# Kernel tuning notes

Measured on AMD Instinct MI355X. Metric: run time of the kernel, lower is better.

The kernel has to match this reference:

```python
import jax, jax.numpy as jnp
import numpy as np

N_NODES, F_IN, HID, HEADS, REP, NCLS = 8192, 128, 64, 8, 512, 32
E, NSYN, LMAX = 2048, 4096, 8
DM, DI, DSTATE, DCONV, DTR = 512, 1024, 16, 4, 32


def setup_inputs():
    key = jax.random.key(0)
    ks = jax.random.split(key, 24)
    g = lambda i, shape, s=0.05: jax.random.normal(ks[i], shape, jnp.float32) * s
    return {
        "edge_attr": jax.random.normal(ks[0], (E, 8), jnp.float32),
        "synapse": jax.random.normal(ks[1], (NSYN, 6), jnp.float32),
        "x_param": g(2, (N_NODES, F_IN), 0.1),
        "W1": g(3, (F_IN, HEADS * HID)),
        "att_src1": g(4, (HEADS, HID), 0.1),
        "att_dst1": g(5, (HEADS, HID), 0.1),
        "b1": jnp.zeros((HEADS * HID,), jnp.float32),
        "W2": g(6, (HEADS * HID, REP)),
        "att_src2": g(7, (1, REP), 0.1),
        "att_dst2": g(8, (1, REP), 0.1),
        "b2": jnp.zeros((REP,), jnp.float32),
        "W_in": g(9, (6, DM), 0.1),
        "b_in": jnp.zeros((DM,), jnp.float32),
        "W_inproj": g(10, (DM, 2 * DI)),
        "conv_w": g(11, (DI, DCONV), 0.1),
        "conv_b": jnp.zeros((DI,), jnp.float32),
        "W_xproj": g(12, (DI, DTR + 2 * DSTATE)),
        "W_dt": g(13, (DTR, DI), 0.1),
        "b_dt": jnp.full((DI,), -4.0, jnp.float32),
        "A_log": jnp.log(jnp.tile(jnp.arange(1, DSTATE + 1, dtype=jnp.float32), (DI, 1))),
        "D": jnp.ones((DI,), jnp.float32),
        "W_outproj": g(14, (DI, DM)),
        "W_lout": g(15, (DM, DM)),
        "b_lout": jnp.zeros((DM,), jnp.float32),
        "Wc1": g(16, (REP + 2 * DM, 512)),
        "bc1": jnp.zeros((512,), jnp.float32),
        "Wc2": g(17, (512, NCLS)),
        "bc2": jnp.zeros((NCLS,), jnp.float32),
        "edge_index": jax.random.randint(ks[18], (2, E), 0, N_NODES),
        "synapse_index": jnp.sort(jax.random.randint(ks[19], (NSYN,), 0, E)),
        "scatter_size": N_NODES,
    }


def _gat(x, W, a_src, a_dst, bias, src, dst, heads, out_ch, concat):
    # PyG GATConv (eval mode, edge_dim=None, self-loops already appended to src/dst)
    n = x.shape[0]
    xw = (x @ W).reshape(n, heads, out_ch)
    e = (xw * a_src).sum(-1)[src] + (xw * a_dst).sum(-1)[dst]  # [E+N, H]
    e = jax.nn.leaky_relu(e, 0.2)
    m = jax.ops.segment_max(e, dst, num_segments=n)
    ex = jnp.exp(e - m[dst])
    denom = jax.ops.segment_sum(ex, dst, num_segments=n)
    alpha = ex / denom[dst]
    out = jax.ops.segment_sum(alpha[:, :, None] * xw[src], dst, num_segments=n)
    out = out.reshape(n, heads * out_ch) if concat else out.mean(1)
    return out + bias


def _mamba_encoder(synapse, synapse_index, W_in, b_in, W_inproj, conv_w, conv_b,
                   W_xproj, W_dt, b_dt, A_log, D, W_outproj, W_lout, b_lout):
    # ragged [NSYN,6] -> padded [E, LMAX, 6] (synapse_index is sorted)
    counts = jax.ops.segment_sum(jnp.ones((NSYN,), jnp.int32), synapse_index, num_segments=E)
    starts = jnp.cumsum(counts) - counts
    pos = jnp.arange(NSYN) - starts[synapse_index]
    padded = jnp.zeros((E, LMAX, synapse.shape[1]), synapse.dtype).at[
        synapse_index, pos].set(synapse, mode="drop")
    u = padded @ W_in + b_in                     # linear_in: [E, L, DM]
    xz = u @ W_inproj                            # in_proj:   [E, L, 2*DI]
    xm, z = xz[..., :DI], xz[..., DI:]
    # depthwise causal conv over time
    xc = jax.lax.conv_general_dilated(
        xm.transpose(0, 2, 1), conv_w[:, None, :],
        window_strides=(1,), padding=[(DCONV - 1, 0)],
        dimension_numbers=("NCH", "OIH", "NCH"), feature_group_count=DI)
    xc = jax.nn.silu(xc + conv_b[:, None]).transpose(0, 2, 1)  # [E, L, DI]
    xdb = xc @ W_xproj
    dt = jax.nn.softplus(xdb[..., :DTR] @ W_dt + b_dt)         # [E, L, DI]
    Bm = xdb[..., DTR:DTR + DSTATE]                            # [E, L, N]
    Cm = xdb[..., DTR + DSTATE:]                               # [E, L, N]
    A = -jnp.exp(A_log)                                        # [DI, N]

    def step(h, t):
        dt_t, B_t, C_t, x_t = t                                # [E,DI],[E,N],[E,N],[E,DI]
        h = jnp.exp(dt_t[:, :, None] * A) * h + (dt_t * x_t)[:, :, None] * B_t[:, None, :]
        return h, jnp.einsum("bdn,bn->bd", h, C_t)

    h0 = jnp.zeros((E, DI, DSTATE), xc.dtype)
    _, ys = jax.lax.scan(step, h0, (dt.transpose(1, 0, 2), Bm.transpose(1, 0, 2),
                                    Cm.transpose(1, 0, 2), xc.transpose(1, 0, 2)))
    y = ys.transpose(1, 0, 2) + D * xc                         # [E, L, DI]
    out = (y * jax.nn.silu(z)) @ W_outproj                     # [E, L, DM]
    # masked mean over true sequence length (empty groups behave like a zero seq of len 1)
    cnt = jnp.clip(counts, 1, LMAX).astype(out.dtype)
    mask = (jnp.arange(LMAX)[None, :] < cnt[:, None]).astype(out.dtype)
    pooled = (out * mask[:, :, None]).sum(1) / cnt[:, None]
    return pooled @ W_lout + b_lout                            # [E, DM]


def _forward(edge_attr, synapse, x_param, W1, att_src1, att_dst1, b1,
             W2, att_src2, att_dst2, b2, W_in, b_in, W_inproj, conv_w, conv_b,
             W_xproj, W_dt, b_dt, A_log, D, W_outproj, W_lout, b_lout,
             Wc1, bc1, Wc2, bc2, edge_index, synapse_index, scatter_size):
    # GAT stack (eval: dropouts identity; edge_attr unused since edge_dim=None)
    loops = jnp.arange(N_NODES)
    src = jnp.concatenate([edge_index[0], loops])
    dst = jnp.concatenate([edge_index[1], loops])
    h = jax.nn.elu(_gat(x_param, W1, att_src1, att_dst1, b1, src, dst, HEADS, HID, True))
    h = _gat(h, W2, att_src2, att_dst2, b2, src, dst, 1, REP, False)   # [N, REP]
    x_point = _mamba_encoder(synapse, synapse_index, W_in, b_in, W_inproj, conv_w,
                             conv_b, W_xproj, W_dt, b_dt, A_log, D, W_outproj,
                             W_lout, b_lout)                            # [E, DM]

    def smax(idx):
        s = jax.ops.segment_max(x_point, idx, num_segments=scatter_size)
        nz = jax.ops.segment_sum(jnp.ones((E,), jnp.int32), idx, num_segments=scatter_size)
        return jnp.where(nz[:, None] > 0, s, 0.0)  # torch_scatter: empty slots -> 0

    left, right = smax(edge_index[0]), smax(edge_index[1])
    feats = jnp.concatenate([h, left, right], axis=1)          # [N, REP+2*DM]
    return jax.nn.relu(feats @ Wc1 + bc1) @ Wc2 + bc2          # [N, NCLS]


def reference(edge_attr, synapse, x_param, W1, att_src1, att_dst1, b1,
              W2, att_src2, att_dst2, b2, W_in, b_in, W_inproj, conv_w, conv_b,
              W_xproj, W_dt, b_dt, A_log, D, W_outproj, W_lout, b_lout,
              Wc1, bc1, Wc2, bc2, edge_index, synapse_index, scatter_size):
    return _forward(edge_attr, synapse, x_param, W1, att_src1, att_dst1, b1,
                    W2, att_src2, att_dst2, b2, W_in, b_in, W_inproj, conv_w, conv_b,
                    W_xproj, W_dt, b_dt, A_log, D, W_outproj, W_lout, b_lout,
                    Wc1, bc1, Wc2, bc2, edge_index, synapse_index, scatter_size)
```

## Files before the change

kernel.cpp:

```cpp
#include <hip/hip_runtime.h>

#define N_NODES 8192
#define F_IN 128
#define HID 64
#define HEADS 8
#define REP 512
#define NCLS 32
#define E_EDGES 2048
#define NSYN 4096
#define LMAX 8
#define DM 512
#define DI 1024
#define DSTATE 16
#define DCONV 4
#define DTR 32
#define TOT_EDGES (E_EDGES + N_NODES)
#define ROWS (E_EDGES * LMAX)
#define MC_CAP 6144

typedef short bf16x8 __attribute__((ext_vector_type(8)));
typedef float f32x4 __attribute__((ext_vector_type(4)));

__device__ __forceinline__ unsigned mapf(float f) {
  unsigned u = __float_as_uint(f);
  return (u & 0x80000000u) ? ~u : (u | 0x80000000u);
}
__device__ __forceinline__ float unmapf(unsigned u) {
  return __uint_as_float((u & 0x80000000u) ? (u ^ 0x80000000u) : ~u);
}
__device__ __forceinline__ float fsig(float x) {
  return __builtin_amdgcn_rcpf(1.0f + __expf(-x));
}
__device__ __forceinline__ float fsoftplus(float x) {
  return fmaxf(x, 0.0f) + __logf(1.0f + __expf(-fabsf(x)));
}
__device__ __forceinline__ unsigned short f2bf(float f) {
  unsigned u = __float_as_uint(f);
  unsigned r = (u + 0x7FFFu + ((u >> 16) & 1u)) >> 16;
  return (unsigned short)r;
}
__device__ __forceinline__ float bf2f(unsigned short h) {
  return __uint_as_float(((unsigned)h) << 16);
}
__device__ __forceinline__ void split2(float x, unsigned short* hh, unsigned short* ll) {
  unsigned short h = f2bf(x);
  *hh = h;
  *ll = f2bf(x - bf2f(h));
}
__device__ __forceinline__ int lower_bound_dev(const int* __restrict__ arr, int n, int v) {
  int lo = 0, hi = n;
  while (lo < hi) { int mid = (lo + hi) >> 1; if (arr[mid] < v) lo = mid + 1; else hi = mid; }
  return lo;
}
__device__ __forceinline__ int src_of(const int* __restrict__ ei, int i) {
  return i < E_EDGES ? ei[i] : i - E_EDGES;
}
__device__ __forceinline__ int dst_of(const int* __restrict__ ei, int i) {
  return i < E_EDGES ? ei[E_EDGES + i] : i - E_EDGES;
}
__device__ __forceinline__ int clip_cnt(int c) { return c < 1 ? 1 : (c > LMAX ? LMAX : c); }

__global__ __launch_bounds__(512) void gemm_mfma2(
    const unsigned short* __restrict__ Ah, const unsigned short* __restrict__ Al,
    const unsigned short* __restrict__ Bth, const unsigned short* __restrict__ Btl,
    float* __restrict__ C, int M, int N, int K,
    const float* __restrict__ bias, int act) {
  __shared__ __align__(16) unsigned short As[2][128][40];
  __shared__ __align__(16) unsigned short Bs[2][128][40];
  const int tid = threadIdx.x;
  const int w = tid >> 6;
  const int lane = tid & 63;
  const int wr = w >> 2, wc = w & 3;
  const int mb = M >> 7;
  const int lin = blockIdx.x;
  const int bx = lin / mb;
  const int by = lin % mb;
  const int brow = by * 128;
  const int bcol = bx * 128;
  const int r0 = lane & 15;
  const int kg = lane >> 4;
  const int row0 = tid >> 2, kc0 = tid & 3;
  const size_t a0 = (size_t)(brow + row0) * K + kc0 * 8;
  const size_t b0 = (size_t)(bcol + row0) * K + kc0 * 8;
  f32x4 acc[4][2] = {};
  {
    bf16x8 t0 = *(const bf16x8*)(Ah + a0), t1 = *(const bf16x8*)(Al + a0);
    bf16x8 t2 = *(const bf16x8*)(Bth + b0), t3 = *(const bf16x8*)(Btl + b0);
    *(bf16x8*)(&As[0][row0][kc0 * 8]) = t0;
    *(bf16x8*)(&As[1][row0][kc0 * 8]) = t1;
    *(bf16x8*)(&Bs[0][row0][kc0 * 8]) = t2;
    *(bf16x8*)(&Bs[1][row0][kc0 * 8]) = t3;
  }
  __syncthreads();
  for (int kt = 0; kt < K; kt += 32) {
    const bool more = (kt + 32) < K;
    bf16x8 p0, p1, p2, p3;
    if (more) {
      p0 = *(const bf16x8*)(Ah + a0 + kt + 32);
      p1 = *(const bf16x8*)(Al + a0 + kt + 32);
      p2 = *(const bf16x8*)(Bth + b0 + kt + 32);
      p3 = *(const bf16x8*)(Btl + b0 + kt + 32);
    }
    bf16x8 bhv[2], blv[2];
#pragma unroll
    for (int cf = 0; cf < 2; ++cf) {
      bhv[cf] = *(const bf16x8*)(&Bs[0][wc * 32 + cf * 16 + r0][kg * 8]);
      blv[cf] = *(const bf16x8*)(&Bs[1][wc * 32 + cf * 16 + r0][kg * 8]);
    }
#pragma unroll
    for (int rf = 0; rf < 4; ++rf) {
      bf16x8 ah = *(const bf16x8*)(&As[0][wr * 64 + rf * 16 + r0][kg * 8]);
      bf16x8 al = *(const bf16x8*)(&As[1][wr * 64 + rf * 16 + r0][kg * 8]);
#pragma unroll
      for (int cf = 0; cf < 2; ++cf) {
        acc[rf][cf] = __builtin_amdgcn_mfma_f32_16x16x32_bf16(ah, bhv[cf], acc[rf][cf], 0, 0, 0);
        acc[rf][cf] = __builtin_amdgcn_mfma_f32_16x16x32_bf16(ah, blv[cf], acc[rf][cf], 0, 0, 0);
        acc[rf][cf] = __builtin_amdgcn_mfma_f32_16x16x32_bf16(al, bhv[cf], acc[rf][cf], 0, 0, 0);
      }
    }
    __syncthreads();
    if (more) {
      *(bf16x8*)(&As[0][row0][kc0 * 8]) = p0;
      *(bf16x8*)(&As[1][row0][kc0 * 8]) = p1;
      *(bf16x8*)(&Bs[0][row0][kc0 * 8]) = p2;
      *(bf16x8*)(&Bs[1][row0][kc0 * 8]) = p3;
    }
    __syncthreads();
  }
#pragma unroll
  for (int rf = 0; rf < 4; ++rf)
#pragma unroll
    for (int cf = 0; cf < 2; ++cf) {
      int col = bcol + wc * 32 + cf * 16 + r0;
      float bb = bias ? bias[col] : 0.0f;
#pragma unroll
      for (int j = 0; j < 4; ++j) {
        int row = brow + wr * 64 + rf * 16 + kg * 4 + j;
        float v = acc[rf][cf][j] + bb;
        if (act == 1) v = fmaxf(v, 0.0f);
        C[(size_t)row * N + col] = v;
      }
    }
}

__global__ __launch_bounds__(256) void gemm_mfma_sk(
    const unsigned short* __restrict__ Ah, const unsigned short* __restrict__ Al,
    const unsigned short* __restrict__ Bth, const unsigned short* __restrict__ Btl,
    float* __restrict__ C, int M, int N, int K) {
  __shared__ __align__(16) unsigned short As[2][64][40];
  const int tid = threadIdx.x;
  const int w = tid >> 6;
  const int lane = tid & 63;
  const int brow = blockIdx.y * 64;
  const int bcol = blockIdx.x * 64;
  const int srow = tid >> 2;
  const int skc = tid & 3;
  const int r0 = lane & 15;
  const int kg = lane >> 4;
  const int kchunk = K / gridDim.z;
  const int k0 = blockIdx.z * kchunk;
  f32x4 acc[4] = {};
  const size_t aoff = (size_t)(brow + srow) * K;
  const size_t boff = (size_t)(bcol + w * 16 + r0) * K + kg * 8;
  for (int kt = k0; kt < k0 + kchunk; kt += 32) {
    bf16x8 bh = *(const bf16x8*)(Bth + boff + kt);
    bf16x8 bl = *(const bf16x8*)(Btl + boff + kt);
    *(bf16x8*)(&As[0][srow][skc * 8]) = *(const bf16x8*)(Ah + aoff + kt + skc * 8);
    *(bf16x8*)(&As[1][srow][skc * 8]) = *(const bf16x8*)(Al + aoff + kt + skc * 8);
    __syncthreads();
#pragma unroll
    for (int r = 0; r < 4; ++r) {
      bf16x8 ah = *(const bf16x8*)(&As[0][r * 16 + r0][kg * 8]);
      bf16x8 al = *(const bf16x8*)(&As[1][r * 16 + r0][kg * 8]);
      acc[r] = __builtin_amdgcn_mfma_f32_16x16x32_bf16(ah, bh, acc[r], 0, 0, 0);
      acc[r] = __builtin_amdgcn_mfma_f32_16x16x32_bf16(ah, bl, acc[r], 0, 0, 0);
      acc[r] = __builtin_amdgcn_mfma_f32_16x16x32_bf16(al, bh, acc[r], 0, 0, 0);
    }
    __syncthreads();
  }
  const int col = bcol + w * 16 + r0;
#pragma unroll
  for (int r = 0; r < 4; ++r) {
#pragma unroll
    for (int j = 0; j < 4; ++j) {
      int row = brow + r * 16 + kg * 4 + j;
      atomicAdd(&C[(size_t)row * N + col], acc[r][j]);
    }
  }
}

template <int APPLY_RELU>
__global__ __launch_bounds__(256) void gemm_thin32(
    const float* __restrict__ A32,
    const unsigned short* __restrict__ Bth, const unsigned short* __restrict__ Btl,
    float* __restrict__ C, int M, const float* __restrict__ bias) {
  const int tid = threadIdx.x;
  const int w = tid >> 6;
  const int lane = tid & 63;
  const int r0 = lane & 15;
  const int kg = lane >> 4;
  const int rowbase = blockIdx.x * 64 + w * 16;
  f32x4 acc[2] = {};
  const float* arow = A32 + (size_t)(rowbase + r0) * 512 + kg * 8;
  for (int kt = 0; kt < 512; kt += 32) {
    float4 f0 = *(const float4*)(arow + kt);
    float4 f1 = *(const float4*)(arow + kt + 4);
    float v[8] = {f0.x, f0.y, f0.z, f0.w, f1.x, f1.y, f1.z, f1.w};
    bf16x8 ah, al;
#pragma unroll
    for (int j = 0; j < 8; ++j) {
      float vv = APPLY_RELU ? fmaxf(v[j], 0.0f) : v[j];
      unsigned short hh, ll;
      split2(vv, &hh, &ll);
      ah[j] = (short)hh;
      al[j] = (short)ll;
    }
#pragma unroll
    for (int cf = 0; cf < 2; ++cf) {
      bf16x8 bh = *(const bf16x8*)(Bth + (size_t)(cf * 16 + r0) * 512 + kt + kg * 8);
      bf16x8 bl = *(const bf16x8*)(Btl + (size_t)(cf * 16 + r0) * 512 + kt + kg * 8);
      acc[cf] = __builtin_amdgcn_mfma_f32_16x16x32_bf16(ah, bh, acc[cf], 0, 0, 0);
      acc[cf] = __builtin_amdgcn_mfma_f32_16x16x32_bf16(ah, bl, acc[cf], 0, 0, 0);
      acc[cf] = __builtin_amdgcn_mfma_f32_16x16x32_bf16(al, bh, acc[cf], 0, 0, 0);
    }
  }
#pragma unroll
  for (int cf = 0; cf < 2; ++cf) {
    int col = cf * 16 + r0;
    float bb = bias[col];
#pragma unroll
    for (int j = 0; j < 4; ++j) {
      int row = rowbase + kg * 4 + j;
      C[(size_t)row * 32 + col] = acc[cf][j] + bb;
    }
  }
}

__global__ void split_kernel(const float* __restrict__ x, unsigned short* __restrict__ h,
                             unsigned short* __restrict__ l, int n) {
  int i = blockIdx.x * 256 + threadIdx.x;
  if (i >= n) return;
  split2(x[i], &h[i], &l[i]);
}

__global__ void tsplit_kernel(const float* __restrict__ W, unsigned short* __restrict__ Wth,
                              unsigned short* __restrict__ Wtl, int K, int N) {
  int i = blockIdx.x * 256 + threadIdx.x;
  if (i >= K * N) return;
  int k = i / N, n = i - k * N;
  float v = W[i];
  unsigned short h = f2bf(v);
  Wth[(size_t)n * K + k] = h;
  Wtl[(size_t)n * K + k] = f2bf(v - bf2f(h));
}

#define PREP_SEG0 262144
#define PREP_SEG1 524288
#define PREP_SEG2 16384
#define PREP_SEG3 65536
#define PREP_SEG4 65536
#define PREP_SEG5 1048576
#define PREP_TOT (PREP_SEG0 + PREP_SEG1 + PREP_SEG2 + PREP_SEG3 + PREP_SEG4 + PREP_SEG5)
__global__ void prep1_kernel(
    const float* __restrict__ W_lout, const float* __restrict__ W_outproj,
    const float* __restrict__ A_log, const float* __restrict__ W_xproj,
    const float* __restrict__ W1, const float* __restrict__ x_param,
    unsigned short* __restrict__ Wlth, unsigned short* __restrict__ Wltl,
    unsigned short* __restrict__ Woph, unsigned short* __restrict__ Wopl,
    float* __restrict__ negA,
    unsigned short* __restrict__ Wxth, unsigned short* __restrict__ Wxtl,
    unsigned short* __restrict__ W1th, unsigned short* __restrict__ W1tl,
    unsigned short* __restrict__ xph, unsigned short* __restrict__ xpl) {
  int i = blockIdx.x * 256 + threadIdx.x;
  if (i < PREP_SEG0) {
    int k = i >> 9, n = i & 511;
    float v = W_lout[i];
    unsigned short h = f2bf(v);
    Wlth[(size_t)n * 512 + k] = h;
    Wltl[(size_t)n * 512 + k] = f2bf(v - bf2f(h));
    return;
  }
  i -= PREP_SEG0;
  if (i < PREP_SEG1) { split2(W_outproj[i], &Woph[i], &Wopl[i]); return; }
  i -= PREP_SEG1;
  if (i < PREP_SEG2) { negA[i] = -__expf(A_log[i]); return; }
  i -= PREP_SEG2;
  if (i < PREP_SEG3) {
    int k = i >> 6, n = i & 63;
    float v = W_xproj[i];
    unsigned short h = f2bf(v);
    Wxth[(size_t)n * 1024 + k] = h;
    Wxtl[(size_t)n * 1024 + k] = f2bf(v - bf2f(h));
    return;
  }
  i -= PREP_SEG3;
  if (i < PREP_SEG4) {
    int k = i >> 9, n = i & 511;
    float v = W1[i];
    unsigned short h = f2bf(v);
    W1th[(size_t)n * 128 + k] = h;
    W1tl[(size_t)n * 128 + k] = f2bf(v - bf2f(h));
    return;
  }
  i -= PREP_SEG4;
  if (i < PREP_SEG5) { split2(x_param[i], &xph[i], &xpl[i]); }
}

template <int BM, int BN>
__global__ __launch_bounds__(256) void gemm_t(
    const float* __restrict__ A, int lda,
    const float* __restrict__ B, int ldb,
    float* __restrict__ C, int ldc,
    int M, int N, int K,
    const float* __restrict__ bias, int act) {
  constexpr int RR = BM / 64;
  constexpr int CR = BN / 64;
  __shared__ float As[16][BM + 4];
  __shared__ float Bs[16][BN + 4];
  const int tid = threadIdx.x;
  const int tx = tid & 15;
  const int ty = tid >> 4;
  const int brow = blockIdx.y * BM;
  const int bcol = blockIdx.x * BN;
  float acc[RR][CR][4][4] = {};
  for (int kt = 0; kt < K; kt += 16) {
#pragma unroll
    for (int p = 0; p < RR; ++p) {
      int c = tid + p * 256;
      int row = c >> 2, kc = c & 3;
      int gr = brow + row;
      float4 v = make_float4(0.f, 0.f, 0.f, 0.f);
      if (gr < M) v = *reinterpret_cast<const float4*>(A + (size_t)gr * lda + kt + kc * 4);
      As[kc * 4 + 0][row] = v.x;
      As[kc * 4 + 1][row] = v.y;
      As[kc * 4 + 2][row] = v.z;
      As[kc * 4 + 3][row] = v.w;
    }
#pragma unroll
    for (int p = 0; p < CR; ++p) {
      int c = tid + p * 256;
      int k = c / (BN / 4), c4 = c % (BN / 4);
      int gc = bcol + c4 * 4;
      float4 v = make_float4(0.f, 0.f, 0.f, 0.f);
      if (gc < N) v = *reinterpret_cast<const float4*>(B + (size_t)(kt + k) * ldb + gc);
      *reinterpret_cast<float4*>(&Bs[k][c4 * 4]) = v;
    }
    __syncthreads();
#pragma unroll
    for (int k = 0; k < 16; ++k) {
      float av[RR * 4], bv[CR * 4];
#pragma unroll
      for (int r = 0; r < RR; ++r) {
        float4 t = *reinterpret_cast<const float4*>(&As[k][r * 64 + ty * 4]);
        av[r * 4 + 0] = t.x; av[r * 4 + 1] = t.y; av[r * 4 + 2] = t.z; av[r * 4 + 3] = t.w;
      }
#pragma unroll
      for (int cq = 0; cq < CR; ++cq) {
        float4 t = *reinterpret_cast<const float4*>(&Bs[k][cq * 64 + tx * 4]);
        bv[cq * 4 + 0] = t.x; bv[cq * 4 + 1] = t.y; bv[cq * 4 + 2] = t.z; bv[cq * 4 + 3] = t.w;
      }
#pragma unroll
      for (int r = 0; r < RR; ++r)
#pragma unroll
        for (int cq = 0; cq < CR; ++cq)
#pragma unroll
          for (int i = 0; i < 4; ++i)
#pragma unroll
            for (int j = 0; j < 4; ++j)
              acc[r][cq][i][j] = fmaf(av[r * 4 + i], bv[cq * 4 + j], acc[r][cq][i][j]);
    }
    __syncthreads();
  }
#pragma unroll
  for (int r = 0; r < RR; ++r)
#pragma unroll
    for (int i = 0; i < 4; ++i) {
      int row = brow + r * 64 + ty * 4 + i;
      if (row >= M) continue;
#pragma unroll
      for (int cq = 0; cq < CR; ++cq) {
        int col = bcol + cq * 64 + tx * 4;
        if (col >= N) continue;
        float4 v;
        v.x = acc[r][cq][i][0]; v.y = acc[r][cq][i][1];
        v.z = acc[r][cq][i][2]; v.w = acc[r][cq][i][3];
        if (bias) {
          float4 bb = *reinterpret_cast<const float4*>(bias + col);
          v.x += bb.x; v.y += bb.y; v.z += bb.z; v.w += bb.w;
        }
        if (act == 1) {
          v.x = fmaxf(v.x, 0.f); v.y = fmaxf(v.y, 0.f);
          v.z = fmaxf(v.z, 0.f); v.w = fmaxf(v.w, 0.f);
        }
        *reinterpret_cast<float4*>(C + (size_t)row * ldc + col) = v;
      }
    }
}

__global__ void scatter_padded_kernel(const float* __restrict__ synapse,
                                      const int* __restrict__ sidx,
                                      float* __restrict__ padded) {
  int i = blockIdx.x * 256 + threadIdx.x;
  if (i >= NSYN) return;
  int e = sidx[i];
  int lo = lower_bound_dev(sidx, NSYN, e);
  int pos = i - lo;
  if (pos < LMAX) {
#pragma unroll
    for (int c = 0; c < 6; ++c) padded[((size_t)e * LMAX + pos) * 6 + c] = synapse[(size_t)i * 6 + c];
  }
}

__global__ __launch_bounds__(256) void prefix_kernel(const int* __restrict__ sidx,
                                                     int* __restrict__ counts,
                                                     int* __restrict__ starts_c) {
  __shared__ int part[256];
  int t = threadIdx.x;
  int loc[8];
  int s = 0;
  int lo = lower_bound_dev(sidx, NSYN, t * 8);
#pragma unroll
  for (int i = 0; i < 8; ++i) {
    int hi = lower_bound_dev(sidx, NSYN, t * 8 + i + 1);
    int c = hi - lo;
    counts[t * 8 + i] = c;
    lo = hi;
    c = clip_cnt(c);
    loc[i] = s;
    s += c;
  }
  part[t] = s;
  __syncthreads();
  int mytot = s;
  for (int o = 1; o < 256; o <<= 1) {
    int add = (t >= o) ? part[t - o] : 0;
    __syncthreads();
    part[t] += add;
    __syncthreads();
  }
  int off = part[t] - mytot;
#pragma unroll
  for (int i = 0; i < 8; ++i) starts_c[t * 8 + i] = off + loc[i];
}

__global__ __launch_bounds__(256) void xc_compact_kernel(
    const float* __restrict__ padded,
    const float* __restrict__ W_eff, const float* __restrict__ b_eff,
    const float* __restrict__ conv_w, const float* __restrict__ conv_b,
    const int* __restrict__ counts, const int* __restrict__ starts_c,
    unsigned short* __restrict__ xch, unsigned short* __restrict__ xcl) {
  __shared__ float pads[LMAX * 6];
  int t = threadIdx.x;
  int d = blockIdx.x * 256 + t;
  int e = blockIdx.y;
  if (t < LMAX * 6) pads[t] = padded[(size_t)e * LMAX * 6 + t];
  __syncthreads();
  int cnt = clip_cnt(counts[e]);
  int sc = starts_c[e];
  float wef[6];
#pragma unroll
  for (int c = 0; c < 6; ++c) wef[c] = W_eff[c * 2048 + d];
  float cw0 = conv_w[d * 4 + 0], cw1 = conv_w[d * 4 + 1];
  float cw2 = conv_w[d * 4 + 2], cw3 = conv_w[d * 4 + 3];
  float cb = conv_b[d], be = b_eff[d];
  float x0 = 0.f, x1 = 0.f, x2 = 0.f;
  for (int l = 0; l < cnt; ++l) {
    float xm = be;
#pragma unroll
    for (int c = 0; c < 6; ++c) xm += pads[l * 6 + c] * wef[c];
    float s0 = cb + xm * cw3;
    if (l >= 1) s0 += x2 * cw2;
    if (l >= 2) s0 += x1 * cw1;
    if (l >= 3) s0 += x0 * cw0;
    float v = s0 * fsig(s0);
    size_t o = (size_t)(sc + l) * DI + d;
    split2(v, &xch[o], &xcl[o]);
    x0 = x1; x1 = x2; x2 = xm;
  }
}

__global__ __launch_bounds__(256) void mamba_scan_pool_kernel(
    const float* __restrict__ xdb_c, const float* __restrict__ padded,
    const float* __restrict__ W_eff, const float* __restrict__ b_eff,
    const float* __restrict__ W_dt, const float* __restrict__ b_dt,
    const float* __restrict__ negA, const float* __restrict__ Dv,
    const float* __restrict__ conv_w, const float* __restrict__ conv_b,
    const int* __restrict__ counts, const int* __restrict__ starts_c,
    unsigned short* __restrict__ pooledh, unsigned short* __restrict__ pooledl) {
  __shared__ float pads[LMAX * 6];
  __shared__ float rows[LMAX * 64];
  int t = threadIdx.x;
  int d = blockIdx.x * 256 + t;
  int e = blockIdx.y;
  int cnt = clip_cnt(counts[e]);
  int sc = starts_c[e];
  if (t < LMAX * 6) pads[t] = padded[(size_t)e * LMAX * 6 + t];
  for (int i = t; i < cnt * 64; i += 256) rows[i] = xdb_c[(size_t)sc * 64 + i];
  float wdt[DTR];
#pragma unroll
  for (int k = 0; k < DTR; ++k) wdt[k] = W_dt[k * DI + d];
  float a[DSTATE];
#pragma unroll
  for (int n = 0; n < DSTATE; ++n) a[n] = negA[d * DSTATE + n];
  float h[DSTATE];
#pragma unroll
  for (int n = 0; n < DSTATE; ++n) h[n] = 0.0f;
  float wef[6], wez[6];
#pragma unroll
  for (int c = 0; c < 6; ++c) {
    wef[c] = W_eff[c * 2048 + d];
    wez[c] = W_eff[c * 2048 + DI + d];
  }
  float cw0 = conv_w[d * 4 + 0], cw1 = conv_w[d * 4 + 1];
  float cw2 = conv_w[d * 4 + 2], cw3 = conv_w[d * 4 + 3];
  float cb = conv_b[d];
  float bdt = b_dt[d], Dd = Dv[d], be = b_eff[d], bez = b_eff[DI + d];
  __syncthreads();
  float x0 = 0.f, x1 = 0.f, x2 = 0.f;
  float ssum = 0.0f;
  for (int l = 0; l < cnt; ++l) {
    float xm = be;
#pragma unroll
    for (int c = 0; c < 6; ++c) xm += pads[l * 6 + c] * wef[c];
    float s0 = cb + xm * cw3;
    if (l >= 1) s0 += x2 * cw2;
    if (l >= 2) s0 += x1 * cw1;
    if (l >= 3) s0 += x0 * cw0;
    float xt = s0 * fsig(s0);
    const float* __restrict__ xrow = &rows[l * 64];
    float acc = bdt;
#pragma unroll
    for (int k = 0; k < DTR; ++k) acc += xrow[k] * wdt[k];
    float dt = fsoftplus(acc);
    float dtx = dt * xt;
    float y = 0.0f;
#pragma unroll
    for (int n = 0; n < DSTATE; ++n) {
      float en = __expf(dt * a[n]);
      h[n] = en * h[n] + dtx * xrow[32 + n];
      y += h[n] * xrow[48 + n];
    }
    y += Dd * xt;
    float z = bez;
#pragma unroll
    for (int c = 0; c < 6; ++c) z += pads[l * 6 + c] * wez[c];
    ssum += y * z * fsig(z);
    x0 = x1; x1 = x2; x2 = xm;
  }
  float pv = ssum / (float)cnt;
  split2(pv, &pooledh[(size_t)e * DI + d], &pooledl[(size_t)e * DI + d]);
}

__global__ void esed1_kernel(const float* __restrict__ xw1, const float* __restrict__ as1,
                             const float* __restrict__ ad1, float* __restrict__ es1,
                             float* __restrict__ ed1) {
  int idx = blockIdx.x * 256 + threadIdx.x;
  int n = idx >> 3, h = idx & 7;
  const float* xr = xw1 + (size_t)n * 512 + h * 64;
  const float* sr = as1 + h * 64;
  const float* dr = ad1 + h * 64;
  float es = 0.0f, ed = 0.0f;
#pragma unroll
  for (int c = 0; c < 64; ++c) { float v = xr[c]; es += v * sr[c]; ed += v * dr[c]; }
  es1[idx] = es; ed1[idx] = ed;
}

__global__ void edgeexp1_kernel(const int* __restrict__ ei, const float* __restrict__ es1,
                                const float* __restrict__ ed1, float* __restrict__ e1,
                                float* __restrict__ denom1) {
  int idx = blockIdx.x * 256 + threadIdx.x;
  if (idx >= TOT_EDGES * HEADS) return;
  int i = idx >> 3, h = idx & 7;
  int s = src_of(ei, i), d = dst_of(ei, i);
  float v = es1[s * 8 + h] + ed1[d * 8 + h];
  v = v >= 0.0f ? v : 0.2f * v;
  float ex = expf(v);
  e1[idx] = ex;
  atomicAdd(denom1 + d * 8 + h, ex);
}

__global__ void selfinit1_kernel(const float* __restrict__ e1, const float* __restrict__ denom1,
                                 const float* __restrict__ xw1, float* __restrict__ g1) {
  int idx = blockIdx.x * 256 + threadIdx.x;
  int n = idx >> 9, j = idx & 511;
  int h = j >> 6;
  float alpha = e1[(size_t)(E_EDGES + n) * 8 + h] / denom1[n * 8 + h];
  g1[idx] = alpha * xw1[idx];
}

__global__ __launch_bounds__(256) void agg1_kernel(const int* __restrict__ ei,
                                                   const float* __restrict__ e1,
                                                   const float* __restrict__ denom1,
                                                   const float* __restrict__ xw1,
                                                   float* __restrict__ g1) {
  int i = blockIdx.x;
  int s = ei[i], d = ei[E_EDGES + i];
  for (int j = threadIdx.x; j < 512; j += 256) {
    int h = j >> 6;
    float alpha = e1[i * 8 + h] / denom1[d * 8 + h];
    atomicAdd(g1 + (size_t)d * 512 + j, alpha * xw1[(size_t)s * 512 + j]);
  }
}

__global__ void elu_bias_split_kernel(const float* __restrict__ g1, const float* __restrict__ b1,
                                      unsigned short* __restrict__ g1h,
                                      unsigned short* __restrict__ g1l) {
  int idx = blockIdx.x * 256 + threadIdx.x;
  int j = idx & 511;
  float v = g1[idx] + b1[j];
  v = v > 0.0f ? v : expm1f(v);
  split2(v, &g1h[idx], &g1l[idx]);
}

__global__ __launch_bounds__(64) void esed2_kernel(const float* __restrict__ xw2,
                                                   const float* __restrict__ as2,
                                                   const float* __restrict__ ad2,
                                                   float* __restrict__ es2,
                                                   float* __restrict__ ed2) {
  int n = blockIdx.x, t = threadIdx.x;
  float es = 0.0f, ed = 0.0f;
  for (int c = t; c < 512; c += 64) {
    float v = xw2[(size_t)n * 512 + c];
    es += v * as2[c]; ed += v * ad2[c];
  }
#pragma unroll
  for (int o = 32; o > 0; o >>= 1) { es += __shfl_down(es, o, 64); ed += __shfl_down(ed, o, 64); }
  if (t == 0) { es2[n] = es; ed2[n] = ed; }
}

__global__ void edgeexp2_kernel(const int* __restrict__ ei, const float* __restrict__ es2,
                                const float* __restrict__ ed2, float* __restrict__ e2,
                                float* __restrict__ denom2) {
  int i = blockIdx.x * 256 + threadIdx.x;
  if (i >= TOT_EDGES) return;
  int s = src_of(ei, i), d = dst_of(ei, i);
  float v = es2[s] + ed2[d];
  v = v >= 0.0f ? v : 0.2f * v;
  float ex = expf(v);
  e2[i] = ex;
  atomicAdd(denom2 + d, ex);
}

__global__ void selfinit2_kernel(const float* __restrict__ e2, const float* __restrict__ denom2,
                                 const float* __restrict__ xw2, float* __restrict__ g2) {
  int idx = blockIdx.x * 256 + threadIdx.x;
  int n = idx >> 9;
  float alpha = e2[E_EDGES + n] / denom2[n];
  g2[idx] = alpha * xw2[idx];
}

__global__ __launch_bounds__(256) void agg2_kernel(const int* __restrict__ ei,
                                                   const float* __restrict__ e2,
                                                   const float* __restrict__ denom2,
                                                   const float* __restrict__ xw2,
                                                   float* __restrict__ g2) {
  int i = blockIdx.x;
  int s = ei[i], d = ei[E_EDGES + i];
  float alpha = e2[i] / denom2[d];
  for (int j = threadIdx.x; j < 512; j += 256) {
    atomicAdd(g2 + (size_t)d * 512 + j, alpha * xw2[(size_t)s * 512 + j]);
  }
}

__global__ __launch_bounds__(256) void leftright_kernel(const int* __restrict__ ei,
                                                        const float* __restrict__ xp,
                                                        const float* __restrict__ b_lout,
                                                        unsigned* __restrict__ leftU,
                                                        unsigned* __restrict__ rightU,
                                                        int* __restrict__ flagL,
                                                        int* __restrict__ flagR) {
  int i = blockIdx.x;
  int s = ei[i], d = ei[E_EDGES + i];
  if (threadIdx.x == 0) { flagL[s] = 1; flagR[d] = 1; }
  for (int j = threadIdx.x; j < 512; j += 256) {
    unsigned v = mapf(xp[(size_t)i * 512 + j] + b_lout[j]);
    atomicMax(leftU + (size_t)s * 512 + j, v);
    atomicMax(rightU + (size_t)d * 512 + j, v);
  }
}

__global__ void concat_split_kernel(const float* __restrict__ g2, const float* __restrict__ b2,
                                    const unsigned* __restrict__ leftU,
                                    const unsigned* __restrict__ rightU,
                                    const int* __restrict__ flagL, const int* __restrict__ flagR,
                                    unsigned short* __restrict__ fh,
                                    unsigned short* __restrict__ fl) {
  int idx = blockIdx.x * 256 + threadIdx.x;
  int n = idx >> 9, j = idx & 511;
  size_t base = (size_t)n * 1536 + j;
  split2(g2[idx] + b2[j], &fh[base], &fl[base]);
  split2(flagL[n] ? unmapf(leftU[idx]) : 0.0f, &fh[base + 512], &fl[base + 512]);
  split2(flagR[n] ? unmapf(rightU[idx]) : 0.0f, &fh[base + 1024], &fl[base + 1024]);
}

extern "C" void kernel_launch(void* const* d_in, const int* in_sizes, int n_in,
                              void* d_out, int out_size, void* d_ws, size_t ws_size,
                              hipStream_t stream) {
  const float* synapse = (const float*)d_in[1];
  const float* x_param = (const float*)d_in[2];
  const float* W1 = (const float*)d_in[3];
  const float* as1 = (const float*)d_in[4];
  const float* ad1 = (const float*)d_in[5];
  const float* b1 = (const float*)d_in[6];
  const float* W2 = (const float*)d_in[7];
  const float* as2 = (const float*)d_in[8];
  const float* ad2 = (const float*)d_in[9];
  const float* b2 = (const float*)d_in[10];
  const float* W_in = (const float*)d_in[11];
  const float* b_in = (const float*)d_in[12];
  const float* W_inproj = (const float*)d_in[13];
  const float* conv_w = (const float*)d_in[14];
  const float* conv_b = (const float*)d_in[15];
  const float* W_xproj = (const float*)d_in[16];
  const float* W_dt = (const float*)d_in[17];
  const float* b_dt = (const float*)d_in[18];
  const float* A_log = (const float*)d_in[19];
  const float* Dv = (const float*)d_in[20];
  const float* W_outproj = (const float*)d_in[21];
  const float* W_lout = (const float*)d_in[22];
  const float* b_lout = (const float*)d_in[23];
  const float* Wc1 = (const float*)d_in[24];
  const float* bc1 = (const float*)d_in[25];
  const float* Wc2 = (const float*)d_in[26];
  const float* bc2 = (const float*)d_in[27];
  const int* edge_index = (const int*)d_in[28];
  const int* sidx = (const int*)d_in[29];
  float* out = (float*)d_out;

  const size_t MB = (size_t)1 << 20;
  const size_t KB = (size_t)1 << 10;
  char* ws = (char*)d_ws;
  unsigned short* xc_ch = (unsigned short*)(ws + 0);
  unsigned short* xc_cl = (unsigned short*)(ws + 16 * MB);
  float* xw1 = (float*)(ws + 0);
  float* g1 = (float*)(ws + 16 * MB);
  unsigned short* g1h = (unsigned short*)(ws + 32 * MB);
  unsigned short* g1l = (unsigned short*)(ws + 40 * MB);
  unsigned short* xph = (unsigned short*)(ws + 48 * MB);
  unsigned short* xpl = (unsigned short*)(ws + 50 * MB);
  unsigned short* W1th = (unsigned short*)(ws + 52 * MB);
  unsigned short* W1tl = (unsigned short*)(ws + 52 * MB + 128 * KB);
  float* xw2 = (float*)(ws + 48 * MB);
  unsigned short* W2th = (unsigned short*)(ws + 0);
  unsigned short* W2tl = (unsigned short*)(ws + 512 * KB);
  float* g2 = (float*)(ws + 0);
  unsigned short* featsh = (unsigned short*)(ws + 16 * MB);
  unsigned short* featsl = (unsigned short*)(ws + 40 * MB);
  float* hidden = (float*)(ws + 0);
  float* xdb_c = (float*)(ws + 64 * MB);
  unsigned short* pooledh = (unsigned short*)(ws + 68 * MB);
  unsigned short* pooledl = (unsigned short*)(ws + 72 * MB);
  unsigned short* Wxth = (unsigned short*)(ws + 76 * MB);
  unsigned short* Wxtl = (unsigned short*)(ws + 76 * MB + 128 * KB);
  float* WmixT = (float*)(ws + 77 * MB);
  unsigned short* Wmixth = (unsigned short*)(ws + 80 * MB);
  unsigned short* Wmixtl = (unsigned short*)(ws + 81 * MB);
  unsigned short* Wlth = (unsigned short*)(ws + 82 * MB);
  unsigned short* Wltl = (unsigned short*)(ws + 82 * MB + 512 * KB);
  unsigned short* Woph = (unsigned short*)(ws + 83 * MB);
  unsigned short* Wopl = (unsigned short*)(ws + 84 * MB);
  float* negA = (float*)(ws + 85 * MB);
  unsigned* leftU = (unsigned*)(ws + 64 * MB);
  unsigned* rightU = (unsigned*)(ws + 80 * MB);
  float* x_point = (float*)(ws + 96 * MB);
  unsigned short* Wc1th = (unsigned short*)(ws + 96 * MB);
  unsigned short* Wc1tl = (unsigned short*)(ws + 96 * MB + 1536 * KB);
  unsigned short* Wc2th = (unsigned short*)(ws + 99 * MB);
  unsigned short* Wc2tl = (unsigned short*)(ws + 99 * MB + 64 * KB);
  char* sm = ws + 100 * MB;
  float* es1 = (float*)(sm + 0);
  float* ed1 = (float*)(sm + 256 * KB);
  float* e1 = (float*)(sm + 512 * KB);
  float* denom1 = (float*)(sm + 1088 * KB);
  float* es2 = (float*)(sm + 1344 * KB);
  float* ed2 = (float*)(sm + 1376 * KB);
  float* e2 = (float*)(sm + 1408 * KB);
  float* denom2 = (float*)(sm + 1480 * KB);
  int* flagL = (int*)(sm + 1512 * KB);
  int* flagR = (int*)(sm + 1544 * KB);
  float* padded = (float*)(ws + 106 * MB);
  int* counts = (int*)(ws + 106 * MB + 384 * KB);
  float* W_eff = (float*)(ws + 106 * MB + 400 * KB);
  float* b_eff = (float*)(ws + 106 * MB + 448 * KB);
  int* starts_c = (int*)(ws + 106 * MB + 456 * KB);

  auto g64 = [&](const float* A, int lda, const float* B, int ldb, float* C, int ldc,
                 int M, int N, int K, const float* bias, int act) {
    dim3 grid((N + 63) / 64, (M + 63) / 64);
    gemm_t<64, 64><<<grid, 256, 0, stream>>>(A, lda, B, ldb, C, ldc, M, N, K, bias, act);
  };
  auto gm2 = [&](const unsigned short* Ah, const unsigned short* Al,
                 const unsigned short* Bth, const unsigned short* Btl, float* C,
                 int M, int N, int K, const float* bias, int act) {
    gemm_mfma2<<<(N / 128) * (M / 128), 512, 0, stream>>>(Ah, Al, Bth, Btl, C, M, N, K, bias,
                                                          act);
  };
  auto tsplit = [&](const float* W, unsigned short* th, unsigned short* tl, int K, int N) {
    tsplit_kernel<<<(K * N + 255) / 256, 256, 0, stream>>>(W, th, tl, K, N);
  };
  auto split = [&](const float* x, unsigned short* h, unsigned short* l, int n) {
    split_kernel<<<(n + 255) / 256, 256, 0, stream>>>(x, h, l, n);
  };

  g64(W_in, DM, W_inproj, 2 * DI, W_eff, 2 * DI, 6, 2 * DI, DM, nullptr, 0);
  g64(b_in, DM, W_inproj, 2 * DI, b_eff, 2 * DI, 1, 2 * DI, DM, nullptr, 0);
  prep1_kernel<<<PREP_TOT / 256, 256, 0, stream>>>(
      W_lout, W_outproj, A_log, W_xproj, W1, x_param,
      Wlth, Wltl, Woph, Wopl, negA, Wxth, Wxtl, W1th, W1tl, xph, xpl);
  hipMemsetAsync(WmixT, 0, (size_t)DM * DI * 4, stream);
  gemm_mfma_sk<<<dim3(DI / 64, DM / 64, 4), 256, 0, stream>>>(Wlth, Wltl, Woph, Wopl, WmixT,
                                                              DM, DI, DM);
  split(WmixT, Wmixth, Wmixtl, DM * DI);

  hipMemsetAsync(padded, 0, (size_t)ROWS * 6 * 4, stream);
  scatter_padded_kernel<<<(NSYN + 255) / 256, 256, 0, stream>>>(synapse, sidx, padded);
  prefix_kernel<<<1, 256, 0, stream>>>(sidx, counts, starts_c);
  xc_compact_kernel<<<dim3(DI / 256, E_EDGES), 256, 0, stream>>>(
      padded, W_eff, b_eff, conv_w, conv_b, counts, starts_c, xc_ch, xc_cl);
  hipMemsetAsync(xdb_c, 0, (size_t)MC_CAP * 64 * 4, stream);
  gemm_mfma_sk<<<dim3(1, MC_CAP / 64, 8), 256, 0, stream>>>(xc_ch, xc_cl, Wxth, Wxtl, xdb_c,
                                                            MC_CAP, 64, DI);
  mamba_scan_pool_kernel<<<dim3(DI / 256, E_EDGES), 256, 0, stream>>>(
      xdb_c, padded, W_eff, b_eff, W_dt, b_dt, negA, Dv, conv_w, conv_b, counts, starts_c,
      pooledh, pooledl);
  hipMemsetAsync(x_point, 0, (size_t)E_EDGES * DM * 4, stream);
  gemm_mfma_sk<<<dim3(DM / 64, E_EDGES / 64, 4), 256, 0, stream>>>(pooledh, pooledl, Wmixth,
                                                                   Wmixtl, x_point, E_EDGES,
                                                                   DM, DI);

  gm2(xph, xpl, W1th, W1tl, xw1, N_NODES, HEADS * HID, F_IN, nullptr, 0);
  esed1_kernel<<<(N_NODES * HEADS) / 256, 256, 0, stream>>>(xw1, as1, ad1, es1, ed1);
  hipMemsetAsync(denom1, 0, 256 * KB, stream);
  edgeexp1_kernel<<<(TOT_EDGES * HEADS + 255) / 256, 256, 0, stream>>>(edge_index, es1, ed1,
                                                                       e1, denom1);
  selfinit1_kernel<<<(N_NODES * 512) / 256, 256, 0, stream>>>(e1, denom1, xw1, g1);
  agg1_kernel<<<E_EDGES, 256, 0, stream>>>(edge_index, e1, denom1, xw1, g1);
  elu_bias_split_kernel<<<(N_NODES * 512) / 256, 256, 0, stream>>>(g1, b1, g1h, g1l);

  tsplit(W2, W2th, W2tl, HEADS * HID, REP);
  gm2(g1h, g1l, W2th, W2tl, xw2, N_NODES, REP, HEADS * HID, nullptr, 0);
  esed2_kernel<<<N_NODES, 64, 0, stream>>>(xw2, as2, ad2, es2, ed2);
  hipMemsetAsync(denom2, 0, 96 * KB, stream);
  edgeexp2_kernel<<<(TOT_EDGES + 255) / 256, 256, 0, stream>>>(edge_index, es2, ed2, e2,
                                                               denom2);
  selfinit2_kernel<<<(N_NODES * 512) / 256, 256, 0, stream>>>(e2, denom2, xw2, g2);
  agg2_kernel<<<E_EDGES, 256, 0, stream>>>(edge_index, e2, denom2, xw2, g2);

  hipMemsetAsync(leftU, 0, 32 * MB, stream);
  leftright_kernel<<<E_EDGES, 256, 0, stream>>>(edge_index, x_point, b_lout, leftU, rightU,
                                                flagL, flagR);

  concat_split_kernel<<<(N_NODES * 512) / 256, 256, 0, stream>>>(g2, b2, leftU, rightU, flagL,
                                                                 flagR, featsh, featsl);
  tsplit(Wc1, Wc1th, Wc1tl, REP + 2 * DM, 512);
  tsplit(Wc2, Wc2th, Wc2tl, 512, NCLS);
  gm2(featsh, featsl, Wc1th, Wc1tl, hidden, N_NODES, 512, REP + 2 * DM, bc1, 1);
  gemm_thin32<0><<<N_NODES / 64, 256, 0, stream>>>(hidden, Wc2th, Wc2tl, out, N_NODES, bc2);
}
```

Baseline: 412.4 us.

## Stage GEMM tiles with direct global-to-LDS loads and double buffering

```diff
diff --git a/kernel.cpp b/kernel.cpp
--- a/kernel.cpp
+++ b/kernel.cpp
@@ -21,6 +21,11 @@
 typedef short bf16x8 __attribute__((ext_vector_type(8)));
 typedef float f32x4 __attribute__((ext_vector_type(4)));
 
+#define GLOAD_LDS16(gp, lp)                                                   \
+  __builtin_amdgcn_global_load_lds(                                           \
+      (const __attribute__((address_space(1))) void*)(gp),                    \
+      (__attribute__((address_space(3))) void*)(lp), 16, 0, 0)
+
 __device__ __forceinline__ unsigned mapf(float f) {
   unsigned u = __float_as_uint(f);
   return (u & 0x80000000u) ? ~u : (u | 0x80000000u);
@@ -65,8 +70,7 @@
     const unsigned short* __restrict__ Bth, const unsigned short* __restrict__ Btl,
     float* __restrict__ C, int M, int N, int K,
     const float* __restrict__ bias, int act) {
-  __shared__ __align__(16) unsigned short As[2][128][40];
-  __shared__ __align__(16) unsigned short Bs[2][128][40];
+  __shared__ __align__(16) unsigned short S[2][4][128][32];
   const int tid = threadIdx.x;
   const int w = tid >> 6;
   const int lane = tid & 63;
@@ -83,47 +87,36 @@
   const size_t a0 = (size_t)(brow + row0) * K + kc0 * 8;
   const size_t b0 = (size_t)(bcol + row0) * K + kc0 * 8;
   f32x4 acc[4][2] = {};
-  {
-    bf16x8 t0 = *(const bf16x8*)(Ah + a0), t1 = *(const bf16x8*)(Al + a0);
-    bf16x8 t2 = *(const bf16x8*)(Bth + b0), t3 = *(const bf16x8*)(Btl + b0);
-    *(bf16x8*)(&As[0][row0][kc0 * 8]) = t0;
-    *(bf16x8*)(&As[1][row0][kc0 * 8]) = t1;
-    *(bf16x8*)(&Bs[0][row0][kc0 * 8]) = t2;
-    *(bf16x8*)(&Bs[1][row0][kc0 * 8]) = t3;
-  }
+
+  auto stage = [&](int buf, int kt) {
+    GLOAD_LDS16(Ah + a0 + kt, &S[buf][0][w * 16][0]);
+    GLOAD_LDS16(Al + a0 + kt, &S[buf][1][w * 16][0]);
+    GLOAD_LDS16(Bth + b0 + kt, &S[buf][2][w * 16][0]);
+    GLOAD_LDS16(Btl + b0 + kt, &S[buf][3][w * 16][0]);
+  };
+
+  stage(0, 0);
   __syncthreads();
-  for (int kt = 0; kt < K; kt += 32) {
-    const bool more = (kt + 32) < K;
-    bf16x8 p0, p1, p2, p3;
-    if (more) {
-      p0 = *(const bf16x8*)(Ah + a0 + kt + 32);
-      p1 = *(const bf16x8*)(Al + a0 + kt + 32);
-      p2 = *(const bf16x8*)(Bth + b0 + kt + 32);
-      p3 = *(const bf16x8*)(Btl + b0 + kt + 32);
-    }
+  const int nk = K >> 5;
+  for (int i = 0; i < nk; ++i) {
+    const int cur = i & 1;
+    if (i + 1 < nk) stage(cur ^ 1, (i + 1) << 5);
     bf16x8 bhv[2], blv[2];
 #pragma unroll
     for (int cf = 0; cf < 2; ++cf) {
-      bhv[cf] = *(const bf16x8*)(&Bs[0][wc * 32 + cf * 16 + r0][kg * 8]);
-      blv[cf] = *(const bf16x8*)(&Bs[1][wc * 32 + cf * 16 + r0][kg * 8]);
+      bhv[cf] = *(const bf16x8*)(&S[cur][2][wc * 32 + cf * 16 + r0][kg * 8]);
+      blv[cf] = *(const bf16x8*)(&S[cur][3][wc * 32 + cf * 16 + r0][kg * 8]);
     }
 #pragma unroll
     for (int rf = 0; rf < 4; ++rf) {
-      bf16x8 ah = *(const bf16x8*)(&As[0][wr * 64 + rf * 16 + r0][kg * 8]);
-      bf16x8 al = *(const bf16x8*)(&As[1][wr * 64 + rf * 16 + r0][kg * 8]);
+      bf16x8 ah = *(const bf16x8*)(&S[cur][0][wr * 64 + rf * 16 + r0][kg * 8]);
+      bf16x8 al = *(const bf16x8*)(&S[cur][1][wr * 64 + rf * 16 + r0][kg * 8]);
 #pragma unroll
       for (int cf = 0; cf < 2; ++cf) {
         acc[rf][cf] = __builtin_amdgcn_mfma_f32_16x16x32_bf16(ah, bhv[cf], acc[rf][cf], 0, 0, 0);
         acc[rf][cf] = __builtin_amdgcn_mfma_f32_16x16x32_bf16(ah, blv[cf], acc[rf][cf], 0, 0, 0);
         acc[rf][cf] = __builtin_amdgcn_mfma_f32_16x16x32_bf16(al, bhv[cf], acc[rf][cf], 0, 0, 0);
       }
-    }
-    __syncthreads();
-    if (more) {
-      *(bf16x8*)(&As[0][row0][kc0 * 8]) = p0;
-      *(bf16x8*)(&As[1][row0][kc0 * 8]) = p1;
-      *(bf16x8*)(&Bs[0][row0][kc0 * 8]) = p2;
-      *(bf16x8*)(&Bs[1][row0][kc0 * 8]) = p3;
     }
     __syncthreads();
   }
```

Result: no change. 410.5 us (-0.5%).
